# Kernel tuning notes

Measured on AMD Instinct MI355X. Metric: run time of the kernel, lower is better.

## Reference

```python
import jax, jax.numpy as jnp
import numpy as np

H, T, D = 16, 4096, 64
N_SEQ = 8  # packed sequences -> cu_seqlens has N_SEQ+1 entries


def setup_inputs() -> dict:
    key = jax.random.key(0)
    kq, kk, kv, kc = jax.random.split(key, 4)
    q = jax.random.normal(kq, (1, H, T, D), dtype=jnp.float32)
    k = jax.random.normal(kk, (1, H, T, D), dtype=jnp.float32)
    v = jax.random.normal(kv, (1, H, T, D), dtype=jnp.float32)
    # cu_seqlens: monotonically increasing offsets, starts at 0, ends at T
    interior = jnp.sort(jax.random.randint(kc, (N_SEQ - 1,), 1, T, dtype=jnp.int32))
    cu_seqlens = jnp.concatenate([
        jnp.zeros((1,), jnp.int32), interior, jnp.full((1,), T, jnp.int32)
    ])
    return {"q": q, "k": k, "v": v, "cu_seqlens": cu_seqlens}


def reference(q, k, v, cu_seqlens):
    # Faithful to flash_attn_varlen_func(..., causal=False) on packed sequences:
    # non-causal attention restricted block-diagonally to each segment.
    scale = 1.0 / jnp.sqrt(jnp.asarray(D, q.dtype))
    # segment id for every token position
    pos = jnp.arange(T)
    seg = jnp.searchsorted(cu_seqlens[1:], pos, side="right")  # [T]
    mask = seg[:, None] == seg[None, :]                         # [T, T] block-diagonal
    # scores: [1, H, T, T]
    scores = jnp.einsum("bhqd,bhkd->bhqk", q, k) * scale
    neg = jnp.asarray(jnp.finfo(scores.dtype).min, scores.dtype)
    scores = jnp.where(mask[None, None], scores, neg)
    attn = jax.nn.softmax(scores, axis=-1)
    out = jnp.einsum("bhqk,bhkd->bhqd", attn, v)  # [1, H, T, D]
    return out
```

## Files before the change

kernel.cpp:

```cpp
#include <hip/hip_runtime.h>

#define HH 16
#define TT 4096
#define DD 64

typedef __attribute__((ext_vector_type(2))) __fp16 half2r;
typedef __attribute__((ext_vector_type(4))) _Float16 half4;
typedef __attribute__((ext_vector_type(8))) _Float16 half8;
typedef __attribute__((ext_vector_type(4))) float float4v;

typedef __attribute__((address_space(3))) unsigned int lds_u32;
typedef __attribute__((address_space(1))) const unsigned int glb_u32;

__global__ __launch_bounds__(256) void pa_prep(
    const float* __restrict__ kg, const float* __restrict__ vg,
    _Float16* __restrict__ k16, _Float16* __restrict__ v16)
{
    __shared__ __align__(16) float Kf[64 * 68];
    __shared__ __align__(16) float Vf[64 * 65];

    const int bid  = blockIdx.x;
    const int h    = bid >> 6;
    const int tile = bid & 63;
    const int kt   = tile << 6;
    const int t    = threadIdx.x;

    const int row = t >> 2, c4 = (t & 3) * 16;
    const float* ksrc = kg + ((size_t)(h * TT) + kt + row) * DD + c4;
    const float* vsrc = vg + ((size_t)(h * TT) + kt + row) * DD + c4;
#pragma unroll
    for (int i = 0; i < 4; ++i) {
        *(float4v*)&Kf[row * 68 + c4 + i * 4] = *(const float4v*)(ksrc + i * 4);
        *(float4v*)&Vf[row * 65 + c4 + i * 4] = *(const float4v*)(vsrc + i * 4);
    }
    __syncthreads();

    char* kdst = (char*)k16 + ((size_t)h * 64 + tile) * 8192;
    char* vdst = (char*)v16 + ((size_t)h * 64 + tile) * 8192;

#pragma unroll
    for (int rep = 0; rep < 2; ++rep) {
        const int idx = t + rep * 256;
        const int r = idx >> 3, s = idx & 7;
        {
            const int sc = s ^ (r & 7);
            float4v a = *(const float4v*)&Kf[r * 68 + sc * 8];
            float4v b = *(const float4v*)&Kf[r * 68 + sc * 8 + 4];
            half2r p0 = __builtin_amdgcn_cvt_pkrtz(a[0], a[1]);
            half2r p1 = __builtin_amdgcn_cvt_pkrtz(a[2], a[3]);
            half2r p2 = __builtin_amdgcn_cvt_pkrtz(b[0], b[1]);
            half2r p3 = __builtin_amdgcn_cvt_pkrtz(b[2], b[3]);
            half8 hk;
            hk[0] = (_Float16)p0[0]; hk[1] = (_Float16)p0[1];
            hk[2] = (_Float16)p1[0]; hk[3] = (_Float16)p1[1];
            hk[4] = (_Float16)p2[0]; hk[5] = (_Float16)p2[1];
            hk[6] = (_Float16)p3[0]; hk[7] = (_Float16)p3[1];
            *(half8*)(kdst + r * 128 + s * 16) = hk;
        }
        {
            const int e  = s ^ (r & 7);
            const int rb = (r >> 3) & 1;
            const int k0 = 8 * e + 4 * rb;
            const int k1 = 8 * e + 4 * (1 - rb);
            float x0 = Vf[(k0 + 0) * 65 + r];
            float x1 = Vf[(k0 + 1) * 65 + r];
            float x2 = Vf[(k0 + 2) * 65 + r];
            float x3 = Vf[(k0 + 3) * 65 + r];
            float y0 = Vf[(k1 + 0) * 65 + r];
            float y1 = Vf[(k1 + 1) * 65 + r];
            float y2 = Vf[(k1 + 2) * 65 + r];
            float y3 = Vf[(k1 + 3) * 65 + r];
            half2r p0 = __builtin_amdgcn_cvt_pkrtz(x0, x1);
            half2r p1 = __builtin_amdgcn_cvt_pkrtz(x2, x3);
            half2r p2 = __builtin_amdgcn_cvt_pkrtz(y0, y1);
            half2r p3 = __builtin_amdgcn_cvt_pkrtz(y2, y3);
            half8 hv;
            hv[0] = (_Float16)p0[0]; hv[1] = (_Float16)p0[1];
            hv[2] = (_Float16)p1[0]; hv[3] = (_Float16)p1[1];
            hv[4] = (_Float16)p2[0]; hv[5] = (_Float16)p2[1];
            hv[6] = (_Float16)p3[0]; hv[7] = (_Float16)p3[1];
            *(half8*)(vdst + r * 128 + s * 16) = hv;
        }
    }
}

__global__ __launch_bounds__(256, 4) void pa_fwd(
    const float* __restrict__ qg, const _Float16* __restrict__ k16,
    const _Float16* __restrict__ v16, const int* __restrict__ cu,
    float* __restrict__ outg)
{
    __shared__ __align__(16) _Float16 Kl[2][64 * 64];
    __shared__ __align__(16) _Float16 Vl[2][64 * 64];

    const int tid  = threadIdx.x;
    const int lane = tid & 63;
    const int wave = tid >> 6;
    const int lr   = lane & 15;
    const int lg   = lane >> 4;

    const int bswz = ((int)blockIdx.x & 7) * 128 + ((int)blockIdx.x >> 3);
    const int h    = bswz >> 6;
    const int qblk = (bswz & 63) << 6;
    const int q    = qblk + wave * 16 + lr;

    int s = 0;
    while (cu[s + 1] <= q) ++s;
    const int lo = cu[s], hi = cu[s + 1];

    int sb = 0;
    while (cu[sb + 1] <= qblk) ++sb;
    const int blo = cu[sb];
    while (cu[sb + 1] <= qblk + 63) ++sb;
    const int bhi = cu[sb + 1];

    const int wlo = __shfl(lo, 0);
    const int whi = __shfl(hi, 15);
    const int mlo = __shfl(lo, 15);
    const int mhi = __shfl(hi, 0);

    const float qscale = 0.125f * 1.44269504088896f;
    const float* qrow = qg + ((size_t)h * TT + q) * DD;
    half8 qf8[2];
#pragma unroll
    for (int ds = 0; ds < 2; ++ds) {
        const float* qp = qrow + ds * 32 + lg * 8;
        float4v a = *(const float4v*)qp;
        float4v b = *(const float4v*)(qp + 4);
        half2r p0 = __builtin_amdgcn_cvt_pkrtz(a[0] * qscale, a[1] * qscale);
        half2r p1 = __builtin_amdgcn_cvt_pkrtz(a[2] * qscale, a[3] * qscale);
        half2r p2 = __builtin_amdgcn_cvt_pkrtz(b[0] * qscale, b[1] * qscale);
        half2r p3 = __builtin_amdgcn_cvt_pkrtz(b[2] * qscale, b[3] * qscale);
        qf8[ds][0] = (_Float16)p0[0]; qf8[ds][1] = (_Float16)p0[1];
        qf8[ds][2] = (_Float16)p1[0]; qf8[ds][3] = (_Float16)p1[1];
        qf8[ds][4] = (_Float16)p2[0]; qf8[ds][5] = (_Float16)p2[1];
        qf8[ds][6] = (_Float16)p3[0]; qf8[ds][7] = (_Float16)p3[1];
    }

    const unsigned kb0 = (unsigned)(lr * 128 + (((lg)     ^ (lr & 7)) << 4));
    const unsigned kb1 = (unsigned)(lr * 128 + (((4 + lg) ^ (lr & 7)) << 4));
    unsigned vrb[4];
#pragma unroll
    for (int t = 0; t < 4; ++t)
        vrb[t] = (unsigned)(lr * 128 + (((2 * t + (lg >> 1)) ^ (lr & 7)) << 4) +
                            (((lg & 1) ^ ((lr >> 3) & 1)) << 3));

    half4 onesv;
    onesv[0] = onesv[1] = onesv[2] = onesv[3] = (_Float16)1.0f;

    const int t0k = blo & ~63;
    const unsigned woff = (unsigned)(wave * 2048 + lane * 16);
    const char* gk = (const char*)k16 + (size_t)h * 524288 + (size_t)t0k * 128 + woff;
    const char* gv = (const char*)v16 + (size_t)h * 524288 + (size_t)t0k * 128 + woff;

#define GLL(CUR)                                                               \
    {                                                                          \
        char* kl = (char*)Kl[CUR] + (wave * 2048);                             \
        char* vl = (char*)Vl[CUR] + (wave * 2048);                             \
        __builtin_amdgcn_global_load_lds((glb_u32*)gk, (lds_u32*)kl, 16, 0, 0);\
        __builtin_amdgcn_global_load_lds((glb_u32*)(gk + 1024),                \
                                         (lds_u32*)(kl + 1024), 16, 0, 0);     \
        __builtin_amdgcn_global_load_lds((glb_u32*)gv, (lds_u32*)vl, 16, 0, 0);\
        __builtin_amdgcn_global_load_lds((glb_u32*)(gv + 1024),                \
                                         (lds_u32*)(vl + 1024), 16, 0, 0);     \
        gk += 8192; gv += 8192;                                                \
    }

    GLL(0);

    float4v acc[4];
#pragma unroll
    for (int dt = 0; dt < 4; ++dt) acc[dt] = (float4v){0.f, 0.f, 0.f, 0.f};
    float4v acc_l = (float4v){0.f, 0.f, 0.f, 0.f};
    float m_run = -1e30f;

    int cur = 0;
    for (int kt = t0k; kt < bhi; kt += 64) {
        asm volatile("s_waitcnt vmcnt(0)" ::: "memory");
        __syncthreads();

        if (kt + 64 < bhi) GLL(cur ^ 1);

        if (!(kt + 64 <= wlo || kt >= whi)) {
            const char* Kb = (const char*)Kl[cur];
            const char* Vb = (const char*)Vl[cur];

            float st[4][4];
            const bool fullv = (kt >= mlo) && (kt + 64 <= mhi);
            __builtin_amdgcn_s_setprio(1);
#pragma unroll
            for (int t = 0; t < 4; ++t) {
                float4v sa = (float4v){0.f, 0.f, 0.f, 0.f};
                half8 kf0 = *(const half8*)(Kb + kb0 + t * 2048);
                half8 kf1 = *(const half8*)(Kb + kb1 + t * 2048);
                sa = __builtin_amdgcn_mfma_f32_16x16x32_f16(kf0, qf8[0], sa, 0, 0, 0);
                sa = __builtin_amdgcn_mfma_f32_16x16x32_f16(kf1, qf8[1], sa, 0, 0, 0);
                if (fullv) {
#pragma unroll
                    for (int j = 0; j < 4; ++j) st[t][j] = sa[j];
                } else {
#pragma unroll
                    for (int j = 0; j < 4; ++j) {
                        const int key = kt + t * 16 + lg * 4 + j;
                        st[t][j] = (key >= lo && key < hi) ? sa[j] : -1e30f;
                    }
                }
            }
            __builtin_amdgcn_s_setprio(0);

            half4 vf01[2][4];
#pragma unroll
            for (int t = 0; t < 2; ++t)
#pragma unroll
                for (int dt = 0; dt < 4; ++dt)
                    vf01[t][dt] = *(const half4*)(Vb + vrb[t] + dt * 2048);

            float lmax = fmaxf(fmaxf(st[0][0], st[0][1]), fmaxf(st[0][2], st[0][3]));
            lmax = fmaxf(lmax, fmaxf(fmaxf(st[1][0], st[1][1]), fmaxf(st[1][2], st[1][3])));
            lmax = fmaxf(lmax, fmaxf(fmaxf(st[2][0], st[2][1]), fmaxf(st[2][2], st[2][3])));
            lmax = fmaxf(lmax, fmaxf(fmaxf(st[3][0], st[3][1]), fmaxf(st[3][2], st[3][3])));

            if (__any(lmax > m_run + 11.54f)) {
                float tx = fmaxf(lmax, __shfl_xor(lmax, 16));
                tx = fmaxf(tx, __shfl_xor(tx, 32));
                const float mn = fmaxf(m_run, tx);
                const float a  = exp2f(m_run - mn);
#pragma unroll
                for (int dt = 0; dt < 4; ++dt)
#pragma unroll
                    for (int j = 0; j < 4; ++j) acc[dt][j] *= a;
#pragma unroll
                for (int j = 0; j < 4; ++j) acc_l[j] *= a;
                m_run = mn;
            }

            half4 pb[4];
#pragma unroll
            for (int t = 0; t < 4; ++t) {
                float e0 = exp2f(st[t][0] - m_run);
                float e1 = exp2f(st[t][1] - m_run);
                float e2 = exp2f(st[t][2] - m_run);
                float e3 = exp2f(st[t][3] - m_run);
                half2r a = __builtin_amdgcn_cvt_pkrtz(e0, e1);
                half2r b = __builtin_amdgcn_cvt_pkrtz(e2, e3);
                pb[t][0] = (_Float16)a[0]; pb[t][1] = (_Float16)a[1];
                pb[t][2] = (_Float16)b[0]; pb[t][3] = (_Float16)b[1];
            }

            __builtin_amdgcn_s_setprio(1);
#pragma unroll
            for (int t = 0; t < 2; ++t) {
#pragma unroll
                for (int dt = 0; dt < 4; ++dt)
                    acc[dt] = __builtin_amdgcn_mfma_f32_16x16x16f16(vf01[t][dt], pb[t], acc[dt], 0, 0, 0);
                acc_l = __builtin_amdgcn_mfma_f32_16x16x16f16(onesv, pb[t], acc_l, 0, 0, 0);
            }
#pragma unroll
            for (int t = 2; t < 4; ++t) {
#pragma unroll
                for (int dt = 0; dt < 4; ++dt) {
                    half4 vf = *(const half4*)(Vb + vrb[t] + dt * 2048);
                    acc[dt] = __builtin_amdgcn_mfma_f32_16x16x16f16(vf, pb[t], acc[dt], 0, 0, 0);
                }
                acc_l = __builtin_amdgcn_mfma_f32_16x16x16f16(onesv, pb[t], acc_l, 0, 0, 0);
            }
            __builtin_amdgcn_s_setprio(0);
        }
        cur ^= 1;
    }

    const float inv = 1.0f / acc_l[0];
    float* orow = outg + ((size_t)h * TT + q) * DD;
#pragma unroll
    for (int dt = 0; dt < 4; ++dt) {
        float4v o;
#pragma unroll
        for (int j = 0; j < 4; ++j) o[j] = acc[dt][j] * inv;
        *(float4v*)(orow + dt * 16 + lg * 4) = o;
    }
#undef GLL
}

extern "C" void kernel_launch(void* const* d_in, const int* in_sizes, int n_in,
                              void* d_out, int out_size, void* d_ws, size_t ws_size,
                              hipStream_t stream) {
    const float* q  = (const float*)d_in[0];
    const float* k  = (const float*)d_in[1];
    const float* v  = (const float*)d_in[2];
    const int*   cu = (const int*)d_in[3];
    float* out = (float*)d_out;

    _Float16* k16 = (_Float16*)d_ws;
    _Float16* v16 = (_Float16*)((char*)d_ws + 8388608);

    dim3 pgrid(HH * 64), pblock(256);
    hipLaunchKernelGGL(pa_prep, pgrid, pblock, 0, stream, k, v, k16, v16);

    dim3 grid(HH * (TT / 64)), block(256);
    hipLaunchKernelGGL(pa_fwd, grid, block, 0, stream, q, k16, v16, cu, out);
}
```

Measured before the change: 81.33 us.

## Read K/V fragments directly from global memory, drop LDS double buffering

Removes the shared-memory double buffer fed by global_load_lds, along with the block-wide barriers. Each wave now loads its K and V MFMA fragments straight from global memory and only loops over its own key range, so waves no longer wait for the block's union range. Occupancy in launch bounds rises from 4 to 8 blocks per CU to hide the longer global latency. The cost is that the four waves no longer share loads of the same tile, so traffic goes through L1/L2 with uncoalesced swizzled reads and no prefetch.

```diff
diff --git a/kernel.cpp b/kernel.cpp
--- a/kernel.cpp
+++ b/kernel.cpp
@@ -8,9 +8,6 @@
 typedef __attribute__((ext_vector_type(4))) _Float16 half4;
 typedef __attribute__((ext_vector_type(8))) _Float16 half8;
 typedef __attribute__((ext_vector_type(4))) float float4v;
-
-typedef __attribute__((address_space(3))) unsigned int lds_u32;
-typedef __attribute__((address_space(1))) const unsigned int glb_u32;
 
 __global__ __launch_bounds__(256) void pa_prep(
     const float* __restrict__ kg, const float* __restrict__ vg,
@@ -84,14 +81,11 @@
     }
 }
 
-__global__ __launch_bounds__(256, 4) void pa_fwd(
+__global__ __launch_bounds__(256, 8) void pa_fwd(
     const float* __restrict__ qg, const _Float16* __restrict__ k16,
     const _Float16* __restrict__ v16, const int* __restrict__ cu,
     float* __restrict__ outg)
 {
-    __shared__ __align__(16) _Float16 Kl[2][64 * 64];
-    __shared__ __align__(16) _Float16 Vl[2][64 * 64];
-
     const int tid  = threadIdx.x;
     const int lane = tid & 63;
     const int wave = tid >> 6;
@@ -106,12 +100,6 @@
     int s = 0;
     while (cu[s + 1] <= q) ++s;
     const int lo = cu[s], hi = cu[s + 1];
-
-    int sb = 0;
-    while (cu[sb + 1] <= qblk) ++sb;
-    const int blo = cu[sb];
-    while (cu[sb + 1] <= qblk + 63) ++sb;
-    const int bhi = cu[sb + 1];
 
     const int wlo = __shfl(lo, 0);
     const int whi = __shfl(hi, 15);
@@ -147,25 +135,8 @@
     half4 onesv;
     onesv[0] = onesv[1] = onesv[2] = onesv[3] = (_Float16)1.0f;
 
-    const int t0k = blo & ~63;
-    const unsigned woff = (unsigned)(wave * 2048 + lane * 16);
-    const char* gk = (const char*)k16 + (size_t)h * 524288 + (size_t)t0k * 128 + woff;
-    const char* gv = (const char*)v16 + (size_t)h * 524288 + (size_t)t0k * 128 + woff;
-
-#define GLL(CUR)                                                               \
-    {                                                                          \
-        char* kl = (char*)Kl[CUR] + (wave * 2048);                             \
-        char* vl = (char*)Vl[CUR] + (wave * 2048);                             \
-        __builtin_amdgcn_global_load_lds((glb_u32*)gk, (lds_u32*)kl, 16, 0, 0);\
-        __builtin_amdgcn_global_load_lds((glb_u32*)(gk + 1024),                \
-                                         (lds_u32*)(kl + 1024), 16, 0, 0);     \
-        __builtin_amdgcn_global_load_lds((glb_u32*)gv, (lds_u32*)vl, 16, 0, 0);\
-        __builtin_amdgcn_global_load_lds((glb_u32*)(gv + 1024),                \
-                                         (lds_u32*)(vl + 1024), 16, 0, 0);     \
-        gk += 8192; gv += 8192;                                                \
-    }
-
-    GLL(0);
+    const char* hk_ = (const char*)k16 + (size_t)h * 524288;
+    const char* hv_ = (const char*)v16 + (size_t)h * 524288;
 
     float4v acc[4];
 #pragma unroll
@@ -173,99 +144,90 @@
     float4v acc_l = (float4v){0.f, 0.f, 0.f, 0.f};
     float m_run = -1e30f;
 
-    int cur = 0;
-    for (int kt = t0k; kt < bhi; kt += 64) {
-        asm volatile("s_waitcnt vmcnt(0)" ::: "memory");
-        __syncthreads();
-
-        if (kt + 64 < bhi) GLL(cur ^ 1);
-
-        if (!(kt + 64 <= wlo || kt >= whi)) {
-            const char* Kb = (const char*)Kl[cur];
-            const char* Vb = (const char*)Vl[cur];
-
-            float st[4][4];
-            const bool fullv = (kt >= mlo) && (kt + 64 <= mhi);
-            __builtin_amdgcn_s_setprio(1);
-#pragma unroll
-            for (int t = 0; t < 4; ++t) {
-                float4v sa = (float4v){0.f, 0.f, 0.f, 0.f};
-                half8 kf0 = *(const half8*)(Kb + kb0 + t * 2048);
-                half8 kf1 = *(const half8*)(Kb + kb1 + t * 2048);
-                sa = __builtin_amdgcn_mfma_f32_16x16x32_f16(kf0, qf8[0], sa, 0, 0, 0);
-                sa = __builtin_amdgcn_mfma_f32_16x16x32_f16(kf1, qf8[1], sa, 0, 0, 0);
-                if (fullv) {
-#pragma unroll
-                    for (int j = 0; j < 4; ++j) st[t][j] = sa[j];
-                } else {
-#pragma unroll
-                    for (int j = 0; j < 4; ++j) {
-                        const int key = kt + t * 16 + lg * 4 + j;
-                        st[t][j] = (key >= lo && key < hi) ? sa[j] : -1e30f;
-                    }
+    for (int kt = wlo & ~63; kt < whi; kt += 64) {
+        const char* Kb = hk_ + (size_t)kt * 128;
+        const char* Vb = hv_ + (size_t)kt * 128;
+
+        float st[4][4];
+        const bool fullv = (kt >= mlo) && (kt + 64 <= mhi);
+        __builtin_amdgcn_s_setprio(1);
+#pragma unroll
+        for (int t = 0; t < 4; ++t) {
+            float4v sa = (float4v){0.f, 0.f, 0.f, 0.f};
+            half8 kf0 = *(const half8*)(Kb + kb0 + t * 2048);
+            half8 kf1 = *(const half8*)(Kb + kb1 + t * 2048);
+            sa = __builtin_amdgcn_mfma_f32_16x16x32_f16(kf0, qf8[0], sa, 0, 0, 0);
+            sa = __builtin_amdgcn_mfma_f32_16x16x32_f16(kf1, qf8[1], sa, 0, 0, 0);
+            if (fullv) {
+#pragma unroll
+                for (int j = 0; j < 4; ++j) st[t][j] = sa[j];
+            } else {
+#pragma unroll
+                for (int j = 0; j < 4; ++j) {
+                    const int key = kt + t * 16 + lg * 4 + j;
+                    st[t][j] = (key >= lo && key < hi) ? sa[j] : -1e30f;
                 }
             }
-            __builtin_amdgcn_s_setprio(0);
-
-            half4 vf01[2][4];
-#pragma unroll
-            for (int t = 0; t < 2; ++t)
-#pragma unroll
-                for (int dt = 0; dt < 4; ++dt)
-                    vf01[t][dt] = *(const half4*)(Vb + vrb[t] + dt * 2048);
-
-            float lmax = fmaxf(fmaxf(st[0][0], st[0][1]), fmaxf(st[0][2], st[0][3]));
-            lmax = fmaxf(lmax, fmaxf(fmaxf(st[1][0], st[1][1]), fmaxf(st[1][2], st[1][3])));
-            lmax = fmaxf(lmax, fmaxf(fmaxf(st[2][0], st[2][1]), fmaxf(st[2][2], st[2][3])));
-            lmax = fmaxf(lmax, fmaxf(fmaxf(st[3][0], st[3][1]), fmaxf(st[3][2], st[3][3])));
-
-            if (__any(lmax > m_run + 11.54f)) {
-                float tx = fmaxf(lmax, __shfl_xor(lmax, 16));
-                tx = fmaxf(tx, __shfl_xor(tx, 32));
-                const float mn = fmaxf(m_run, tx);
-                const float a  = exp2f(m_run - mn);
-#pragma unroll
-                for (int dt = 0; dt < 4; ++dt)
-#pragma unroll
-                    for (int j = 0; j < 4; ++j) acc[dt][j] *= a;
-#pragma unroll
-                for (int j = 0; j < 4; ++j) acc_l[j] *= a;
-                m_run = mn;
+        }
+        __builtin_amdgcn_s_setprio(0);
+
+        half4 vf01[2][4];
+#pragma unroll
+        for (int t = 0; t < 2; ++t)
+#pragma unroll
+            for (int dt = 0; dt < 4; ++dt)
+                vf01[t][dt] = *(const half4*)(Vb + vrb[t] + dt * 2048);
+
+        float lmax = fmaxf(fmaxf(st[0][0], st[0][1]), fmaxf(st[0][2], st[0][3]));
+        lmax = fmaxf(lmax, fmaxf(fmaxf(st[1][0], st[1][1]), fmaxf(st[1][2], st[1][3])));
+        lmax = fmaxf(lmax, fmaxf(fmaxf(st[2][0], st[2][1]), fmaxf(st[2][2], st[2][3])));
+        lmax = fmaxf(lmax, fmaxf(fmaxf(st[3][0], st[3][1]), fmaxf(st[3][2], st[3][3])));
+
+        if (__any(lmax > m_run + 11.54f)) {
+            float tx = fmaxf(lmax, __shfl_xor(lmax, 16));
+            tx = fmaxf(tx, __shfl_xor(tx, 32));
+            const float mn = fmaxf(m_run, tx);
+            const float a  = exp2f(m_run - mn);
+#pragma unroll
+            for (int dt = 0; dt < 4; ++dt)
+#pragma unroll
+                for (int j = 0; j < 4; ++j) acc[dt][j] *= a;
+#pragma unroll
+            for (int j = 0; j < 4; ++j) acc_l[j] *= a;
+            m_run = mn;
+        }
+
+        half4 pb[4];
+#pragma unroll
+        for (int t = 0; t < 4; ++t) {
+            float e0 = exp2f(st[t][0] - m_run);
+            float e1 = exp2f(st[t][1] - m_run);
+            float e2 = exp2f(st[t][2] - m_run);
+            float e3 = exp2f(st[t][3] - m_run);
+            half2r a = __builtin_amdgcn_cvt_pkrtz(e0, e1);
+            half2r b = __builtin_amdgcn_cvt_pkrtz(e2, e3);
+            pb[t][0] = (_Float16)a[0]; pb[t][1] = (_Float16)a[1];
+            pb[t][2] = (_Float16)b[0]; pb[t][3] = (_Float16)b[1];
+        }
+
+        __builtin_amdgcn_s_setprio(1);
+#pragma unroll
+        for (int t = 0; t < 2; ++t) {
+#pragma unroll
+            for (int dt = 0; dt < 4; ++dt)
+                acc[dt] = __builtin_amdgcn_mfma_f32_16x16x16f16(vf01[t][dt], pb[t], acc[dt], 0, 0, 0);
+            acc_l = __builtin_amdgcn_mfma_f32_16x16x16f16(onesv, pb[t], acc_l, 0, 0, 0);
+        }
+#pragma unroll
+        for (int t = 2; t < 4; ++t) {
+#pragma unroll
+            for (int dt = 0; dt < 4; ++dt) {
+                half4 vf = *(const half4*)(Vb + vrb[t] + dt * 2048);
+                acc[dt] = __builtin_amdgcn_mfma_f32_16x16x16f16(vf, pb[t], acc[dt], 0, 0, 0);
             }
-
-            half4 pb[4];
-#pragma unroll
-            for (int t = 0; t < 4; ++t) {
-                float e0 = exp2f(st[t][0] - m_run);
-                float e1 = exp2f(st[t][1] - m_run);
-                float e2 = exp2f(st[t][2] - m_run);
-                float e3 = exp2f(st[t][3] - m_run);
-                half2r a = __builtin_amdgcn_cvt_pkrtz(e0, e1);
-                half2r b = __builtin_amdgcn_cvt_pkrtz(e2, e3);
-                pb[t][0] = (_Float16)a[0]; pb[t][1] = (_Float16)a[1];
-                pb[t][2] = (_Float16)b[0]; pb[t][3] = (_Float16)b[1];
-            }
-
-            __builtin_amdgcn_s_setprio(1);
-#pragma unroll
-            for (int t = 0; t < 2; ++t) {
-#pragma unroll
-                for (int dt = 0; dt < 4; ++dt)
-                    acc[dt] = __builtin_amdgcn_mfma_f32_16x16x16f16(vf01[t][dt], pb[t], acc[dt], 0, 0, 0);
-                acc_l = __builtin_amdgcn_mfma_f32_16x16x16f16(onesv, pb[t], acc_l, 0, 0, 0);
-            }
-#pragma unroll
-            for (int t = 2; t < 4; ++t) {
-#pragma unroll
-                for (int dt = 0; dt < 4; ++dt) {
-                    half4 vf = *(const half4*)(Vb + vrb[t] + dt * 2048);
-                    acc[dt] = __builtin_amdgcn_mfma_f32_16x16x16f16(vf, pb[t], acc[dt], 0, 0, 0);
-                }
-                acc_l = __builtin_amdgcn_mfma_f32_16x16x16f16(onesv, pb[t], acc_l, 0, 0, 0);
-            }
-            __builtin_amdgcn_s_setprio(0);
-        }
-        cur ^= 1;
+            acc_l = __builtin_amdgcn_mfma_f32_16x16x16f16(onesv, pb[t], acc_l, 0, 0, 0);
+        }
+        __builtin_amdgcn_s_setprio(0);
     }
 
     const float inv = 1.0f / acc_l[0];
@@ -277,7 +239,6 @@
         for (int j = 0; j < 4; ++j) o[j] = acc[dt][j] * inv;
         *(float4v*)(orow + dt * 16 + lg * 4) = o;
     }
-#undef GLL
 }
 
 extern "C" void kernel_launch(void* const* d_in, const int* in_sizes, int n_in,
```

After: 277.4 us. +241.0%, slower.
